# Optimization experiments

Measured on AMD Instinct MI355X. Metric: run time of the kernel, lower is better.

The kernel has to match this reference:

```python
import jax, jax.numpy as jnp
import numpy as np

ALPHA = 0.2  # LeakyReLU negative slope used throughout
NEG = -9e15


def _leaky(x, a=ALPHA):
    return jnp.where(x >= 0, x, a * x)


def _gat_layer(h, adj, W, a, concat):
    # h: [N, Fin], W: [Fin, Fout], a: [2*Fout, 1]
    Wh = h @ W                                   # [N, Fout]
    d = W.shape[-1]
    e = _leaky(Wh @ a[:d] + (Wh @ a[d:]).T)      # [N, N]
    att = jax.nn.softmax(jnp.where(adj > 0, e, NEG), axis=1)
    out = att @ Wh                               # [N, Fout]
    return jax.nn.elu(out) if concat else out


def setup_inputs() -> dict:
    key = jax.random.key(0)
    ks = jax.random.split(key, 24)
    N, F, H, D1, O1 = 4096, 512, 4, 256, 64
    x = jax.random.normal(ks[0], (N, F), dtype=jnp.float32)
    adj = jax.random.bernoulli(ks[1], 0.02, (N, N))
    adj = (adj | adj.T | jnp.eye(N, dtype=bool)).astype(jnp.float32)
    observation = jax.random.randint(ks[2], (1, N), 0, 2, dtype=jnp.int32)
    s_mat = jax.random.uniform(ks[3], (N, N), dtype=jnp.float32)
    theta = jax.random.uniform(ks[4], (1, F), dtype=jnp.float32)
    g = lambda k, s, sc: (jax.random.normal(k, s, dtype=jnp.float32) * sc)
    return {
        'x': x, 'adj': adj, 'observation': observation, 's_mat': s_mat,
        'theta': theta,
        'Wh0': g(ks[5], (H, F, D1), 0.05), 'ah0': g(ks[6], (H, 2 * D1, 1), 0.05),
        'Wh1': g(ks[7], (H, D1, D1), 0.05), 'ah1': g(ks[8], (H, 2 * D1, 1), 0.05),
        'Wo0': g(ks[9], (H * D1, O1), 0.05), 'ao0': g(ks[10], (2 * O1, 1), 0.05),
        'Wo1': g(ks[11], (O1, 1), 0.2), 'ao1': g(ks[12], (2, 1), 0.2),
        'dW': g(ks[13], (2, 10), 0.5), 'dW0': g(ks[14], (1, 10), 0.5),
        'dW1': g(ks[15], (10, 20), 0.5), 'dW01': g(ks[16], (1, 20), 0.5),
        'dW2': g(ks[17], (20, 10), 0.5), 'dW02': g(ks[18], (1, 10), 0.5),
        'dV': g(ks[19], (10, 1), 0.5), 'dV0': g(ks[20], (1, 1), 0.5),
    }


def reference(x, adj, observation, s_mat, theta, Wh0, ah0, Wh1, ah1,
              Wo0, ao0, Wo1, ao1, dW, dW0, dW1, dW01, dW2, dW02, dV, dV0):
    # mergeState: add theta to rows in the seed set (observation[0] == 1)
    seed = (observation[0] == 1).astype(x.dtype)[:, None]  # [N,1]
    h_in = x + seed * theta

    # multi-head 2-layer attention stacks (concat=True -> elu inside)
    def head(W0, a0, W1, a1):
        h = _gat_layer(h_in, adj, W0, a0, True)
        return _gat_layer(h, adj, W1, a1, True)

    hh = jax.vmap(head)(Wh0, ah0, Wh1, ah1)                 # [H, N, D1]
    hcat = jnp.transpose(hh, (1, 0, 2)).reshape(h_in.shape[0], -1)  # [N, H*D1]

    # output attention stack (concat=False), then elu (GAT.forward)
    h = _gat_layer(hcat, adj, Wo0, ao0, False)
    h = _gat_layer(h, adj, Wo1, ao1, False)
    h_ = jax.nn.elu(h)                                      # [N, 1]

    # GAT_degree v2: degreeNN over [h_, degree]
    d_v = s_mat.sum(axis=1, keepdims=True)                  # [N, 1]
    x_ = jnp.concatenate([h_, d_v], axis=1)                 # [N, 2]
    h0 = _leaky(x_ @ dW + dW0)
    h1 = _leaky(h0 @ dW1 + dW01)
    h2 = _leaky(h1 @ dW2 + dW02)
    return _leaky(h2 @ dV + dV0)                            # [N, 1]
```

## Files before the change

kernel.cpp:

```cpp
#include <hip/hip_runtime.h>
#include <hip/hip_bf16.h>
#include <hip/hip_fp16.h>
#include <math.h>

#define MAXDEG 512

typedef short v8s __attribute__((ext_vector_type(8)));
typedef float v4f __attribute__((ext_vector_type(4)));
typedef _Float16 h2 __attribute__((ext_vector_type(2)));

__device__ __forceinline__ float blockReduceSum(float v) {
    __shared__ float sh[8];
    int lane = threadIdx.x & 63, w = threadIdx.x >> 6;
    for (int o = 32; o > 0; o >>= 1) v += __shfl_down(v, o);
    __syncthreads();
    if (lane == 0) sh[w] = v;
    __syncthreads();
    if (w == 0) {
        int nw = (blockDim.x + 63) >> 6;
        v = (lane < nw) ? sh[lane] : 0.f;
        for (int o = 4; o > 0; o >>= 1) v += __shfl_down(v, o);
        if (lane == 0) sh[0] = v;
    }
    __syncthreads();
    return sh[0];
}

__device__ __forceinline__ float blockReduceMax(float v) {
    __shared__ float sh[8];
    int lane = threadIdx.x & 63, w = threadIdx.x >> 6;
    for (int o = 32; o > 0; o >>= 1) v = fmaxf(v, __shfl_down(v, o));
    __syncthreads();
    if (lane == 0) sh[w] = v;
    __syncthreads();
    if (w == 0) {
        int nw = (blockDim.x + 63) >> 6;
        v = (lane < nw) ? sh[lane] : -3.4e38f;
        for (int o = 4; o > 0; o >>= 1) v = fmaxf(v, __shfl_down(v, o));
        if (lane == 0) sh[0] = v;
    }
    __syncthreads();
    return sh[0];
}

__device__ __forceinline__ float leaky(float x) { return x >= 0.f ? x : 0.2f * x; }


__global__ void fused_pre(const float* __restrict__ adj, const float* __restrict__ s,
                          int* __restrict__ colIdx, int* __restrict__ deg,
                          float* __restrict__ dv,
                          const float* __restrict__ x, const int* __restrict__ obs,
                          const float* __restrict__ theta,
                          const float* __restrict__ Wh0, const float* __restrict__ Wh1,
                          const float* __restrict__ Wo0,
                          __half* __restrict__ hin, __half* __restrict__ Wh0t,
                          __half* __restrict__ Wh1t, __half* __restrict__ Wo0t,
                          float* __restrict__ elerZ, int elerN, int N) {
    if (blockIdx.x < 4096) {
        int row = blockIdx.x;
        __shared__ int cnt;
        if (threadIdx.x == 0) cnt = 0;
        __syncthreads();
        const float4* ar = (const float4*)(adj + (size_t)row * N);
        const float4* sr = (const float4*)(s + (size_t)row * N);
        int* outp = colIdx + (size_t)row * MAXDEG;
        float psum = 0.f;
        const int n4 = N >> 2;
        for (int j4 = threadIdx.x; j4 < n4; j4 += blockDim.x) {
            float4 a4 = ar[j4];
            float4 s4 = sr[j4];
            psum += (s4.x + s4.y) + (s4.z + s4.w);
            int jb = j4 << 2;
            if (a4.x > 0.f) { int p = atomicAdd(&cnt, 1); if (p < MAXDEG) outp[p] = jb; }
            if (a4.y > 0.f) { int p = atomicAdd(&cnt, 1); if (p < MAXDEG) outp[p] = jb + 1; }
            if (a4.z > 0.f) { int p = atomicAdd(&cnt, 1); if (p < MAXDEG) outp[p] = jb + 2; }
            if (a4.w > 0.f) { int p = atomicAdd(&cnt, 1); if (p < MAXDEG) outp[p] = jb + 3; }
        }
        psum = blockReduceSum(psum);
        __syncthreads();
        if (threadIdx.x == 0) {
            deg[row] = cnt < MAXDEG ? cnt : MAXDEG;
            dv[row] = psum;
        }
        return;
    }
    const int n0 = 4096 * 512;
    const int n1 = 4 * 512 * 256;
    const int n2 = 4 * 256 * 256;
    const int n3 = 1024 * 64;
    int i = (blockIdx.x - 4096) * 256 + threadIdx.x;
    if (i < n0) {
        int n = i >> 9, f = i & 511;
        float v = x[i];
        if (obs[n] == 1) v += theta[f];
        hin[i] = __float2half(v);
    } else if (i < n0 + n1) {
        int t = i - n0;
        int b = t / (512 * 256), r = t % (512 * 256);
        int mm = r >> 9, kk = r & 511;
        Wh0t[t] = __float2half(Wh0[b * 512 * 256 + kk * 256 + mm]);
    } else if (i < n0 + n1 + n2) {
        int t = i - n0 - n1;
        int b = t >> 16, r = t & 65535;
        int mm = r >> 8, kk = r & 255;
        Wh1t[t] = __float2half(Wh1[b * 65536 + kk * 256 + mm]);
    } else if (i < n0 + n1 + n2 + n3) {
        int t = i - n0 - n1 - n2;
        int mm = t >> 10, kk = t & 1023;
        Wo0t[t] = __float2half(Wo0[kk * 64 + mm]);
    } else if (i < n0 + n1 + n2 + n3 + elerN) {
        elerZ[i - n0 - n1 - n2 - n3] = 0.f;
    }
}

__global__ __launch_bounds__(256) void gemm_mfma128(
    const __half* __restrict__ A, const __half* __restrict__ Bt,
    __half* __restrict__ C, int N, int K, int M,
    size_t sA, size_t sB, size_t sC,
    const float* __restrict__ aVec, size_t aStride,
    float* __restrict__ el, float* __restrict__ er) {
    int b = blockIdx.z;
    const unsigned short* Ag = (const unsigned short*)(A + (size_t)b * sA);
    const unsigned short* Bg = (const unsigned short*)(Bt + (size_t)b * sB);
    __half* Cg = C + (size_t)b * sC;
    const float* av = aVec + (size_t)b * aStride;

    __shared__ __align__(16) unsigned short As[128][40];
    __shared__ __align__(16) unsigned short Bs[128][40];

    const int tid = threadIdx.x;
    const int wave = tid >> 6, lane = tid & 63;
    const int wm = wave >> 1, wn = wave & 1;
    const int row0 = blockIdx.y * 128, col0 = blockIdx.x * 128;
    const int lr = tid >> 2;
    const int lo = (tid & 3) * 8;
    const int m = lane & 15, quad = lane >> 4;

    v4f acc[4][4];
    #pragma unroll
    for (int i = 0; i < 4; i++)
        #pragma unroll
        for (int c = 0; c < 4; c++) acc[i][c] = (v4f)(0.f);

    for (int k0 = 0; k0 < K; k0 += 32) {
        *(int4*)(&As[lr][lo]) =
            *(const int4*)(Ag + (size_t)(row0 + lr) * K + k0 + lo);
        *(int4*)(&As[lr + 64][lo]) =
            *(const int4*)(Ag + (size_t)(row0 + 64 + lr) * K + k0 + lo);
        *(int4*)(&Bs[lr][lo]) =
            *(const int4*)(Bg + (size_t)(col0 + lr) * K + k0 + lo);
        *(int4*)(&Bs[lr + 64][lo]) =
            *(const int4*)(Bg + (size_t)(col0 + 64 + lr) * K + k0 + lo);
        __syncthreads();
        v8s af[4], bfv[4];
        #pragma unroll
        for (int i = 0; i < 4; i++)
            af[i] = *(const v8s*)(&As[wm * 64 + i * 16 + m][quad * 8]);
        #pragma unroll
        for (int c = 0; c < 4; c++)
            bfv[c] = *(const v8s*)(&Bs[wn * 64 + c * 16 + m][quad * 8]);
        #pragma unroll
        for (int i = 0; i < 4; i++)
            #pragma unroll
            for (int c = 0; c < 4; c++)
                acc[i][c] = __builtin_amdgcn_mfma_f32_16x16x32_f16(
                    af[i], bfv[c], acc[i][c], 0, 0, 0);
        __syncthreads();
    }
    #pragma unroll
    for (int i = 0; i < 4; i++)
        #pragma unroll
        for (int c = 0; c < 4; c++)
            #pragma unroll
            for (int r = 0; r < 4; r++) {
                int row = row0 + wm * 64 + i * 16 + quad * 4 + r;
                int col = col0 + wn * 64 + c * 16 + m;
                Cg[(size_t)row * M + col] = __float2half(acc[i][c][r]);
            }
    float ael[4], aer[4];
    #pragma unroll
    for (int c = 0; c < 4; c++) {
        ael[c] = av[col0 + wn * 64 + c * 16 + m];
        aer[c] = av[M + col0 + wn * 64 + c * 16 + m];
    }
    #pragma unroll
    for (int i = 0; i < 4; i++)
        #pragma unroll
        for (int r = 0; r < 4; r++) {
            float pel = 0.f, per_ = 0.f;
            #pragma unroll
            for (int c = 0; c < 4; c++) {
                pel += acc[i][c][r] * ael[c];
                per_ += acc[i][c][r] * aer[c];
            }
            #pragma unroll
            for (int off = 1; off < 16; off <<= 1) {
                pel += __shfl_xor(pel, off);
                per_ += __shfl_xor(per_, off);
            }
            if (m == 0) {
                int row = row0 + wm * 64 + i * 16 + quad * 4 + r;
                atomicAdd(&el[(size_t)b * N + row], pel);
                atomicAdd(&er[(size_t)b * N + row], per_);
            }
        }
}

__global__ __launch_bounds__(256) void gemm_mfma64(
    const __half* __restrict__ A, const __half* __restrict__ Bt,
    __half* __restrict__ C, int N, int K, int M,
    size_t sA, size_t sB, size_t sC,
    const float* __restrict__ aVec, size_t aStride,
    float* __restrict__ el, float* __restrict__ er) {
    int b = blockIdx.z;
    const unsigned short* Ag = (const unsigned short*)(A + (size_t)b * sA);
    const unsigned short* Bg = (const unsigned short*)(Bt + (size_t)b * sB);
    __half* Cg = C + (size_t)b * sC;
    const float* av = aVec + (size_t)b * aStride;

    __shared__ __align__(16) unsigned short As[64][40];
    __shared__ __align__(16) unsigned short Bs[64][40];

    const int tid = threadIdx.x;
    const int wave = tid >> 6, lane = tid & 63;
    const int row0 = blockIdx.y * 64, col0 = blockIdx.x * 64;
    const int sRow = tid >> 2;
    const int sOff = (tid & 3) * 8;
    const int m = lane & 15, quad = lane >> 4;

    v4f acc[4];
    #pragma unroll
    for (int c = 0; c < 4; c++) acc[c] = (v4f)(0.f);

    for (int k0 = 0; k0 < K; k0 += 32) {
        *(int4*)(&As[sRow][sOff]) =
            *(const int4*)(Ag + (size_t)(row0 + sRow) * K + k0 + sOff);
        *(int4*)(&Bs[sRow][sOff]) =
            *(const int4*)(Bg + (size_t)(col0 + sRow) * K + k0 + sOff);
        __syncthreads();
        v8s af = *(const v8s*)(&As[wave * 16 + m][quad * 8]);
        #pragma unroll
        for (int c = 0; c < 4; c++) {
            v8s bfv = *(const v8s*)(&Bs[c * 16 + m][quad * 8]);
            acc[c] = __builtin_amdgcn_mfma_f32_16x16x32_f16(af, bfv, acc[c], 0, 0, 0);
        }
        __syncthreads();
    }
    #pragma unroll
    for (int c = 0; c < 4; c++)
        #pragma unroll
        for (int r = 0; r < 4; r++) {
            int row = row0 + wave * 16 + quad * 4 + r;
            int col = col0 + c * 16 + m;
            Cg[(size_t)row * M + col] = __float2half(acc[c][r]);
        }
    float ael[4], aer[4];
    #pragma unroll
    for (int c = 0; c < 4; c++) {
        ael[c] = av[col0 + c * 16 + m];
        aer[c] = av[M + col0 + c * 16 + m];
    }
    #pragma unroll
    for (int r = 0; r < 4; r++) {
        float pel = 0.f, per_ = 0.f;
        #pragma unroll
        for (int c = 0; c < 4; c++) {
            pel += acc[c][r] * ael[c];
            per_ += acc[c][r] * aer[c];
        }
        #pragma unroll
        for (int off = 1; off < 16; off <<= 1) {
            pel += __shfl_xor(pel, off);
            per_ += __shfl_xor(per_, off);
        }
        if (m == 0) {
            int row = row0 + wave * 16 + quad * 4 + r;
            atomicAdd(&el[(size_t)b * N + row], pel);
            atomicAdd(&er[(size_t)b * N + row], per_);
        }
    }
}

template<int D, int ACT, int HEADS, int FUSE>
__global__ __launch_bounds__(256) void attn_vec(
    const __half* __restrict__ Wh, const float* __restrict__ el,
    const float* __restrict__ er, const int* __restrict__ colIdx,
    const int* __restrict__ deg, __half* __restrict__ out,
    int N, size_t sWh, size_t sOut, int outRowStride,
    const float* __restrict__ wo1, const float* __restrict__ ao1,
    float* __restrict__ o2wh, float* __restrict__ el4, float* __restrict__ er4) {
    constexpr int LPN = D / 8;
    constexpr int SUBS = 64 / LPN;
    constexpr int PER_WAVE = SUBS * 4;
    constexpr int STEP = PER_WAVE * 2;

    const int tid = threadIdx.x;
    const int wave = tid >> 6, lane = tid & 63;
    int b, row;
    if (HEADS == 4) {
        int xcd = blockIdx.x & 7;
        b = xcd >> 1;
        row = ((xcd & 1) << 11) + ((blockIdx.x >> 3) << 2) + wave;
    } else {
        b = 0;
        row = blockIdx.x * 4 + wave;
    }

    const __half* whb = Wh + (size_t)b * sWh;
    const float* erb = er + (size_t)b * N;
    const float eln = el[(size_t)b * N + row];
    const int dc = deg[row];
    const int dcp = (dc + STEP - 1) & ~(STEP - 1);
    const int* ci = colIdx + (size_t)row * MAXDEG;

    __shared__ __align__(16) float2 spc[4][MAXDEG];
    float2* sp = spc[wave];

    float sreg[8];
    int jreg[8];
    float mx = -3.4e38f;
    #pragma unroll
    for (int s8 = 0; s8 < 8; s8++) {
        int k = s8 * 64 + lane;
        if (k < dc) {
            int j = ci[k];
            float s = eln + erb[j];
            s = fmaxf(s, 0.2f * s);
            sreg[s8] = s;
            jreg[s8] = j * (D * 2);
            mx = fmaxf(mx, s);
        }
    }
    #pragma unroll
    for (int off = 1; off < 64; off <<= 1) mx = fmaxf(mx, __shfl_xor(mx, off));

    float l = 0.f;
    #pragma unroll
    for (int s8 = 0; s8 < 8; s8++) {
        int k = s8 * 64 + lane;
        if (k < dc) {
            float p = __expf(sreg[s8] - mx);
            l += p;
            unsigned int pu = __half_as_ushort(__float2half(p));
            sp[k] = make_float2(__int_as_float(pu | (pu << 16)),
                                __int_as_float(jreg[s8]));
        }
    }
    for (int k = dc + lane; k < dcp; k += 64)
        sp[k] = make_float2(__int_as_float(0), __int_as_float(0));
    #pragma unroll
    for (int off = 1; off < 64; off <<= 1) l += __shfl_xor(l, off);
    const float inv = 1.f / l;

    asm volatile("s_waitcnt lgkmcnt(0)" ::: "memory");

    const int sub = lane / LPN;
    const int dl = (lane % LPN) * 8;
    const char* wp = (const char*)(whb + dl);

    union HU { unsigned int u; h2 h; };
    union R4 { uint4 u; h2 h[4]; };

    h2 a0[4], a1[4], a2[4], a3[4];
    #pragma unroll
    for (int i = 0; i < 4; i++) {
        a0[i] = (h2)(_Float16)0; a1[i] = (h2)(_Float16)0;
        a2[i] = (h2)(_Float16)0; a3[i] = (h2)(_Float16)0;
    }

    for (int k = sub * 4; k < dcp; k += STEP) {
        float4 pA = *(const float4*)(&sp[k]);
        float4 pB = *(const float4*)(&sp[k + 2]);
        float4 pC = *(const float4*)(&sp[k + PER_WAVE]);
        float4 pD = *(const float4*)(&sp[k + PER_WAVE + 2]);
        R4 r0, r1, r2, r3, r4, r5, r6, r7;
        r0.u = *(const uint4*)(wp + __float_as_int(pA.y));
        r1.u = *(const uint4*)(wp + __float_as_int(pA.w));
        r2.u = *(const uint4*)(wp + __float_as_int(pB.y));
        r3.u = *(const uint4*)(wp + __float_as_int(pB.w));
        r4.u = *(const uint4*)(wp + __float_as_int(pC.y));
        r5.u = *(const uint4*)(wp + __float_as_int(pC.w));
        r6.u = *(const uint4*)(wp + __float_as_int(pD.y));
        r7.u = *(const uint4*)(wp + __float_as_int(pD.w));
        HU p0, p1, p2, p3, p4, p5, p6, p7;
        p0.u = __float_as_int(pA.x);
        p1.u = __float_as_int(pA.z);
        p2.u = __float_as_int(pB.x);
        p3.u = __float_as_int(pB.z);
        p4.u = __float_as_int(pC.x);
        p5.u = __float_as_int(pC.z);
        p6.u = __float_as_int(pD.x);
        p7.u = __float_as_int(pD.z);
        #pragma unroll
        for (int i = 0; i < 4; i++) {
            a0[i] += p0.h * r0.h[i];
            a1[i] += p2.h * r2.h[i];
            a2[i] += p4.h * r4.h[i];
            a3[i] += p6.h * r6.h[i];
        }
        #pragma unroll
        for (int i = 0; i < 4; i++) {
            a0[i] += p1.h * r1.h[i];
            a1[i] += p3.h * r3.h[i];
            a2[i] += p5.h * r5.h[i];
            a3[i] += p7.h * r7.h[i];
        }
    }
    #pragma unroll
    for (int i = 0; i < 4; i++) a0[i] += (a1[i] + (a2[i] + a3[i]));
    #pragma unroll
    for (int off = LPN; off < 64; off <<= 1)
        #pragma unroll
        for (int i = 0; i < 4; i++) {
            HU t, s;
            t.h = a0[i];
            s.u = __shfl_xor((int)t.u, off);
            a0[i] += s.h;
        }

    if (FUSE) {
        if (sub == 0) {
            float t = 0.f;
            #pragma unroll
            for (int i = 0; i < 4; i++) {
                t += (float)a0[i][0] * inv * wo1[dl + 2 * i];
                t += (float)a0[i][1] * inv * wo1[dl + 2 * i + 1];
            }
            #pragma unroll
            for (int off = 1; off < LPN; off <<= 1) t += __shfl_xor(t, off);
            if (lane == 0) {
                o2wh[row] = t;
                el4[row] = t * ao1[0];
                er4[row] = t * ao1[1];
            }
        }
        return;
    }
    if (sub == 0) {
        __half hv[8];
        #pragma unroll
        for (int i = 0; i < 4; i++) {
            float v0 = (float)a0[i][0] * inv;
            float v1 = (float)a0[i][1] * inv;
            if (ACT == 1) {
                v0 = (v0 > 0.f) ? v0 : expm1f(v0);
                v1 = (v1 > 0.f) ? v1 : expm1f(v1);
            }
            hv[2 * i]     = __float2half(v0);
            hv[2 * i + 1] = __float2half(v1);
        }
        *(uint4*)(out + (size_t)b * sOut + (size_t)row * outRowStride + dl) =
            *(const uint4*)hv;
    }
}

__global__ void attn_d1_deg(const float* __restrict__ o2wh, const float* __restrict__ el,
                            const float* __restrict__ er, const int* __restrict__ colIdx,
                            const int* __restrict__ deg, const float* __restrict__ dv,
                            const float* __restrict__ dW, const float* __restrict__ dW0,
                            const float* __restrict__ dW1, const float* __restrict__ dW01,
                            const float* __restrict__ dW2, const float* __restrict__ dW02,
                            const float* __restrict__ dV, const float* __restrict__ dV0,
                            float* __restrict__ out, int N) {
    int row = blockIdx.x, tid = threadIdx.x;
    const float eln = el[row];
    const int dc = deg[row];
    const int* ci = colIdx + (size_t)row * MAXDEG;
    __shared__ float sp[MAXDEG];
    __shared__ int sc[MAXDEG];
    float mx = -3.4e38f;
    for (int k = tid; k < dc; k += blockDim.x) {
        int j = ci[k];
        sc[k] = j;
        float s = eln + er[j];
        s = fmaxf(s, 0.2f * s);
        sp[k] = s;
        mx = fmaxf(mx, s);
    }
    mx = blockReduceMax(mx);
    float l = 0.f, acc = 0.f;
    for (int k = tid; k < dc; k += blockDim.x) {
        float p = __expf(sp[k] - mx);
        l += p;
        acc += p * o2wh[sc[k]];
    }
    l = blockReduceSum(l);
    acc = blockReduceSum(acc);
    if (tid == 0) {
        float h = acc / l;
        h = (h > 0.f) ? h : expm1f(h);
        float d = dv[row];
        float t0[10], t1[20], t2[10];
        #pragma unroll
        for (int i = 0; i < 10; i++)
            t0[i] = leaky(h * dW[i] + d * dW[10 + i] + dW0[i]);
        #pragma unroll
        for (int j = 0; j < 20; j++) {
            float s = dW01[j];
            #pragma unroll
            for (int i = 0; i < 10; i++) s += t0[i] * dW1[i * 20 + j];
            t1[j] = leaky(s);
        }
        #pragma unroll
        for (int j = 0; j < 10; j++) {
            float s = dW02[j];
            #pragma unroll
            for (int i = 0; i < 20; i++) s += t1[i] * dW2[i * 10 + j];
            t2[j] = leaky(s);
        }
        float o = dV0[0];
        #pragma unroll
        for (int i = 0; i < 10; i++) o += t2[i] * dV[i];
        out[row] = leaky(o);
    }
}

extern "C" void kernel_launch(void* const* d_in, const int* in_sizes, int n_in,
                              void* d_out, int out_size, void* d_ws, size_t ws_size,
                              hipStream_t stream) {
    const int N = 4096, F = 512, H = 4, D1 = 256, O1 = 64;
    const float* x     = (const float*)d_in[0];
    const float* adj   = (const float*)d_in[1];
    const int*   obs   = (const int*)  d_in[2];
    const float* s_mat = (const float*)d_in[3];
    const float* theta = (const float*)d_in[4];
    const float* Wh0   = (const float*)d_in[5];
    const float* ah0   = (const float*)d_in[6];
    const float* Wh1   = (const float*)d_in[7];
    const float* ah1   = (const float*)d_in[8];
    const float* Wo0   = (const float*)d_in[9];
    const float* ao0   = (const float*)d_in[10];
    const float* Wo1   = (const float*)d_in[11];
    const float* ao1   = (const float*)d_in[12];
    const float* dWp   = (const float*)d_in[13];
    const float* dW0p  = (const float*)d_in[14];
    const float* dW1p  = (const float*)d_in[15];
    const float* dW01p = (const float*)d_in[16];
    const float* dW2p  = (const float*)d_in[17];
    const float* dW02p = (const float*)d_in[18];
    const float* dVp   = (const float*)d_in[19];
    const float* dV0p  = (const float*)d_in[20];
    float* outp = (float*)d_out;

    char* ws = (char*)d_ws;
    auto alloc = [&](size_t bytes) {
        char* p = ws;
        ws += (bytes + 255) & ~(size_t)255;
        return p;
    };
    __half* hin  = (__half*)alloc((size_t)N * F * 2);
    __half* whA  = (__half*)alloc((size_t)H * N * D1 * 2);
    __half* hb   = (__half*)alloc((size_t)H * N * D1 * 2);
    __half* hcat = (__half*)alloc((size_t)N * H * D1 * 2);
    __half* o1Wh = (__half*)alloc((size_t)N * O1 * 2);
    float* o2Wh  = (float*)alloc((size_t)N * 4);
    __half* Wh0t = (__half*)alloc((size_t)H * F * D1 * 2);
    __half* Wh1t = (__half*)alloc((size_t)H * D1 * D1 * 2);
    __half* Wo0t = (__half*)alloc((size_t)H * D1 * O1 * 2);
    int elerN = 4 * H * N + 2 * N;
    float* elerZ = (float*)alloc((size_t)elerN * 4);
    float* el1 = elerZ;
    float* er1 = el1 + H * N;
    float* el2 = er1 + H * N;
    float* er2 = el2 + H * N;
    float* el3 = er2 + H * N;
    float* er3 = el3 + N;
    float* el4 = (float*)alloc((size_t)N * 4);
    float* er4 = (float*)alloc((size_t)N * 4);
    float* dv  = (float*)alloc((size_t)N * 4);
    int* colIdx = (int*)alloc((size_t)N * MAXDEG * 4);
    int* deg    = (int*)alloc((size_t)N * 4);

    {
        const int totalPrep = N * F + H * F * D1 + H * D1 * D1 + H * D1 * O1 + elerN;
        const int prepBlocks = (totalPrep + 255) / 256;
        fused_pre<<<4096 + prepBlocks, 256, 0, stream>>>(
            adj, s_mat, colIdx, deg, dv,
            x, obs, theta, Wh0, Wh1, Wo0, hin, Wh0t, Wh1t, Wo0t, elerZ, elerN, N);
    }

    gemm_mfma128<<<dim3(D1 / 128, N / 128, H), 256, 0, stream>>>(
        hin, Wh0t, whA, N, F, D1, 0, (size_t)D1 * F, (size_t)N * D1,
        ah0, (size_t)2 * D1, el1, er1);
    attn_vec<256, 1, 4, 0><<<(N * H) / 4, 256, 0, stream>>>(
        whA, el1, er1, colIdx, deg, hb,
        N, (size_t)N * D1, (size_t)N * D1, D1,
        nullptr, nullptr, nullptr, nullptr, nullptr);

    gemm_mfma128<<<dim3(D1 / 128, N / 128, H), 256, 0, stream>>>(
        hb, Wh1t, whA, N, D1, D1, (size_t)N * D1, (size_t)D1 * D1, (size_t)N * D1,
        ah1, (size_t)2 * D1, el2, er2);
    attn_vec<256, 1, 4, 0><<<(N * H) / 4, 256, 0, stream>>>(
        whA, el2, er2, colIdx, deg, hcat,
        N, (size_t)N * D1, (size_t)D1, H * D1,
        nullptr, nullptr, nullptr, nullptr, nullptr);

    gemm_mfma64<<<dim3(O1 / 64, N / 64, 1), 256, 0, stream>>>(
        hcat, Wo0t, o1Wh, N, H * D1, O1, 0, 0, 0,
        ao0, 0, el3, er3);
    attn_vec<64, 0, 1, 1><<<N / 4, 256, 0, stream>>>(
        o1Wh, el3, er3, colIdx, deg, nullptr,
        N, 0, 0, O1,
        Wo1, ao1, o2Wh, el4, er4);

    attn_d1_deg<<<N, 256, 0, stream>>>(o2Wh, el4, er4, colIdx, deg, dv,
        dWp, dW0p, dW1p, dW01p, dW2p, dW02p, dVp, dV0p, outp, N);
}
```

Measured before the change: 389.9 us.

## Use 64x128 GEMM tiles and LDS-tiled weight transposes in prep kernel

The head GEMMs switch from 128x128 to 64x128 block tiles. Each wave now computes 16 rows by 128 columns, and the grid doubles in the row dimension, which raises block count and occupancy for these fairly small GEMMs. The weight transpose-and-convert in the prep kernel moves from strided per-element gathers to 64x64 shared-memory tiles with coalesced float4 loads and 16-byte half stores. The trade-off is less A/B reuse per block, plus extra el/er atomics because each block now covers fewer columns per row.

```diff
diff --git a/kernel.cpp b/kernel.cpp
--- a/kernel.cpp
+++ b/kernel.cpp
@@ -56,17 +56,18 @@
                           __half* __restrict__ hin, __half* __restrict__ Wh0t,
                           __half* __restrict__ Wh1t, __half* __restrict__ Wo0t,
                           float* __restrict__ elerZ, int elerN, int N) {
+    const int tid = threadIdx.x;
     if (blockIdx.x < 4096) {
         int row = blockIdx.x;
         __shared__ int cnt;
-        if (threadIdx.x == 0) cnt = 0;
+        if (tid == 0) cnt = 0;
         __syncthreads();
         const float4* ar = (const float4*)(adj + (size_t)row * N);
         const float4* sr = (const float4*)(s + (size_t)row * N);
         int* outp = colIdx + (size_t)row * MAXDEG;
         float psum = 0.f;
         const int n4 = N >> 2;
-        for (int j4 = threadIdx.x; j4 < n4; j4 += blockDim.x) {
+        for (int j4 = tid; j4 < n4; j4 += blockDim.x) {
             float4 a4 = ar[j4];
             float4 s4 = sr[j4];
             psum += (s4.x + s4.y) + (s4.z + s4.w);
@@ -78,42 +79,73 @@
         }
         psum = blockReduceSum(psum);
         __syncthreads();
-        if (threadIdx.x == 0) {
+        if (tid == 0) {
             deg[row] = cnt < MAXDEG ? cnt : MAXDEG;
             dv[row] = psum;
         }
         return;
     }
-    const int n0 = 4096 * 512;
-    const int n1 = 4 * 512 * 256;
-    const int n2 = 4 * 256 * 256;
-    const int n3 = 1024 * 64;
-    int i = (blockIdx.x - 4096) * 256 + threadIdx.x;
-    if (i < n0) {
+    int bb = blockIdx.x - 4096;
+    if (bb < 8192) {
+        int i = bb * 256 + tid;
         int n = i >> 9, f = i & 511;
         float v = x[i];
         if (obs[n] == 1) v += theta[f];
         hin[i] = __float2half(v);
-    } else if (i < n0 + n1) {
-        int t = i - n0;
-        int b = t / (512 * 256), r = t % (512 * 256);
-        int mm = r >> 9, kk = r & 511;
-        Wh0t[t] = __float2half(Wh0[b * 512 * 256 + kk * 256 + mm]);
-    } else if (i < n0 + n1 + n2) {
-        int t = i - n0 - n1;
-        int b = t >> 16, r = t & 65535;
-        int mm = r >> 8, kk = r & 255;
-        Wh1t[t] = __float2half(Wh1[b * 65536 + kk * 256 + mm]);
-    } else if (i < n0 + n1 + n2 + n3) {
-        int t = i - n0 - n1 - n2;
-        int mm = t >> 10, kk = t & 1023;
-        Wo0t[t] = __float2half(Wo0[kk * 64 + mm]);
-    } else if (i < n0 + n1 + n2 + n3 + elerN) {
-        elerZ[i - n0 - n1 - n2 - n3] = 0.f;
-    }
-}
-
-__global__ __launch_bounds__(256) void gemm_mfma128(
+        return;
+    }
+    bb -= 8192;
+    if (bb < 288) {
+        int i = bb * 256 + tid;
+        if (i < elerN) elerZ[i] = 0.f;
+        return;
+    }
+    int t = bb - 288;
+    const float* src;
+    __half* dst;
+    int srcStride, dstStride;
+    if (t < 128) {
+        int b = t >> 5, tt = t & 31, kt = tt >> 2, mt = tt & 3;
+        src = Wh0 + b * 131072 + (kt * 64) * 256 + mt * 64;
+        dst = Wh0t + b * 131072 + (mt * 64) * 512 + kt * 64;
+        srcStride = 256; dstStride = 512;
+    } else if (t < 192) {
+        int u = t - 128;
+        int b = u >> 4, tt = u & 15, kt = tt >> 2, mt = tt & 3;
+        src = Wh1 + b * 65536 + (kt * 64) * 256 + mt * 64;
+        dst = Wh1t + b * 65536 + (mt * 64) * 256 + kt * 64;
+        srcStride = 256; dstStride = 256;
+    } else {
+        int kt = t - 192;
+        src = Wo0 + (kt * 64) * 64;
+        dst = Wo0t + kt * 64;
+        srcStride = 64; dstStride = 1024;
+    }
+    __shared__ float tile[64][65];
+    int rr = tid >> 4;
+    int cc = (tid & 15) * 4;
+    #pragma unroll
+    for (int sI = 0; sI < 4; sI++) {
+        float4 v = *(const float4*)(src + (size_t)(rr + sI * 16) * srcStride + cc);
+        tile[rr + sI * 16][cc]     = v.x;
+        tile[rr + sI * 16][cc + 1] = v.y;
+        tile[rr + sI * 16][cc + 2] = v.z;
+        tile[rr + sI * 16][cc + 3] = v.w;
+    }
+    __syncthreads();
+    int mr = tid >> 2;
+    int kc = (tid & 3) * 16;
+    #pragma unroll
+    for (int g = 0; g < 2; g++) {
+        v8s v;
+        #pragma unroll
+        for (int e = 0; e < 8; e++)
+            v[e] = (short)__half_as_ushort(__float2half(tile[kc + g * 8 + e][mr]));
+        *(v8s*)(dst + (size_t)mr * dstStride + kc + g * 8) = v;
+    }
+}
+
+__global__ __launch_bounds__(256) void gemm_mfma64x128(
     const __half* __restrict__ A, const __half* __restrict__ Bt,
     __half* __restrict__ C, int N, int K, int M,
     size_t sA, size_t sB, size_t sC,
@@ -125,85 +157,69 @@
     __half* Cg = C + (size_t)b * sC;
     const float* av = aVec + (size_t)b * aStride;
 
-    __shared__ __align__(16) unsigned short As[128][40];
+    __shared__ __align__(16) unsigned short As[64][40];
     __shared__ __align__(16) unsigned short Bs[128][40];
 
     const int tid = threadIdx.x;
     const int wave = tid >> 6, lane = tid & 63;
-    const int wm = wave >> 1, wn = wave & 1;
-    const int row0 = blockIdx.y * 128, col0 = blockIdx.x * 128;
+    const int row0 = blockIdx.y * 64, col0 = blockIdx.x * 128;
     const int lr = tid >> 2;
     const int lo = (tid & 3) * 8;
     const int m = lane & 15, quad = lane >> 4;
 
-    v4f acc[4][4];
-    #pragma unroll
-    for (int i = 0; i < 4; i++)
-        #pragma unroll
-        for (int c = 0; c < 4; c++) acc[i][c] = (v4f)(0.f);
+    v4f acc[8];
+    #pragma unroll
+    for (int c = 0; c < 8; c++) acc[c] = (v4f)(0.f);
 
     for (int k0 = 0; k0 < K; k0 += 32) {
         *(int4*)(&As[lr][lo]) =
             *(const int4*)(Ag + (size_t)(row0 + lr) * K + k0 + lo);
-        *(int4*)(&As[lr + 64][lo]) =
-            *(const int4*)(Ag + (size_t)(row0 + 64 + lr) * K + k0 + lo);
         *(int4*)(&Bs[lr][lo]) =
             *(const int4*)(Bg + (size_t)(col0 + lr) * K + k0 + lo);
         *(int4*)(&Bs[lr + 64][lo]) =
             *(const int4*)(Bg + (size_t)(col0 + 64 + lr) * K + k0 + lo);
         __syncthreads();
-        v8s af[4], bfv[4];
-        #pragma unroll
-        for (int i = 0; i < 4; i++)
-            af[i] = *(const v8s*)(&As[wm * 64 + i * 16 + m][quad * 8]);
-        #pragma unroll
-        for (int c = 0; c < 4; c++)
-            bfv[c] = *(const v8s*)(&Bs[wn * 64 + c * 16 + m][quad * 8]);
-        #pragma unroll
-        for (int i = 0; i < 4; i++)
-            #pragma unroll
-            for (int c = 0; c < 4; c++)
-                acc[i][c] = __builtin_amdgcn_mfma_f32_16x16x32_f16(
-                    af[i], bfv[c], acc[i][c], 0, 0, 0);
+        v8s af = *(const v8s*)(&As[wave * 16 + m][quad * 8]);
+        #pragma unroll
+        for (int c = 0; c < 8; c++) {
+            v8s bfv = *(const v8s*)(&Bs[c * 16 + m][quad * 8]);
+            acc[c] = __builtin_amdgcn_mfma_f32_16x16x32_f16(af, bfv, acc[c], 0, 0, 0);
+        }
         __syncthreads();
     }
     #pragma unroll
-    for (int i = 0; i < 4; i++)
-        #pragma unroll
-        for (int c = 0; c < 4; c++)
-            #pragma unroll
-            for (int r = 0; r < 4; r++) {
-                int row = row0 + wm * 64 + i * 16 + quad * 4 + r;
-                int col = col0 + wn * 64 + c * 16 + m;
-                Cg[(size_t)row * M + col] = __float2half(acc[i][c][r]);
-            }
-    float ael[4], aer[4];
-    #pragma unroll
-    for (int c = 0; c < 4; c++) {
-        ael[c] = av[col0 + wn * 64 + c * 16 + m];
-        aer[c] = av[M + col0 + wn * 64 + c * 16 + m];
-    }
-    #pragma unroll
-    for (int i = 0; i < 4; i++)
+    for (int c = 0; c < 8; c++)
         #pragma unroll
         for (int r = 0; r < 4; r++) {
-            float pel = 0.f, per_ = 0.f;
-            #pragma unroll
-            for (int c = 0; c < 4; c++) {
-                pel += acc[i][c][r] * ael[c];
-                per_ += acc[i][c][r] * aer[c];
-            }
-            #pragma unroll
-            for (int off = 1; off < 16; off <<= 1) {
-                pel += __shfl_xor(pel, off);
-                per_ += __shfl_xor(per_, off);
-            }
-            if (m == 0) {
-                int row = row0 + wm * 64 + i * 16 + quad * 4 + r;
-                atomicAdd(&el[(size_t)b * N + row], pel);
-                atomicAdd(&er[(size_t)b * N + row], per_);
-            }
-        }
+            int row = row0 + wave * 16 + quad * 4 + r;
+            int col = col0 + c * 16 + m;
+            Cg[(size_t)row * M + col] = __float2half(acc[c][r]);
+        }
+    float ael[8], aer[8];
+    #pragma unroll
+    for (int c = 0; c < 8; c++) {
+        ael[c] = av[col0 + c * 16 + m];
+        aer[c] = av[M + col0 + c * 16 + m];
+    }
+    #pragma unroll
+    for (int r = 0; r < 4; r++) {
+        float pel = 0.f, per_ = 0.f;
+        #pragma unroll
+        for (int c = 0; c < 8; c++) {
+            pel += acc[c][r] * ael[c];
+            per_ += acc[c][r] * aer[c];
+        }
+        #pragma unroll
+        for (int off = 1; off < 16; off <<= 1) {
+            pel += __shfl_xor(pel, off);
+            per_ += __shfl_xor(per_, off);
+        }
+        if (m == 0) {
+            int row = row0 + wave * 16 + quad * 4 + r;
+            atomicAdd(&el[(size_t)b * N + row], pel);
+            atomicAdd(&er[(size_t)b * N + row], per_);
+        }
+    }
 }
 
 __global__ __launch_bounds__(256) void gemm_mfma64(
@@ -572,14 +588,12 @@
     int* deg    = (int*)alloc((size_t)N * 4);
 
     {
-        const int totalPrep = N * F + H * F * D1 + H * D1 * D1 + H * D1 * O1 + elerN;
-        const int prepBlocks = (totalPrep + 255) / 256;
-        fused_pre<<<4096 + prepBlocks, 256, 0, stream>>>(
+        fused_pre<<<4096 + 8192 + 288 + 208, 256, 0, stream>>>(
             adj, s_mat, colIdx, deg, dv,
             x, obs, theta, Wh0, Wh1, Wo0, hin, Wh0t, Wh1t, Wo0t, elerZ, elerN, N);
     }
 
-    gemm_mfma128<<<dim3(D1 / 128, N / 128, H), 256, 0, stream>>>(
+    gemm_mfma64x128<<<dim3(D1 / 128, N / 64, H), 256, 0, stream>>>(
         hin, Wh0t, whA, N, F, D1, 0, (size_t)D1 * F, (size_t)N * D1,
         ah0, (size_t)2 * D1, el1, er1);
     attn_vec<256, 1, 4, 0><<<(N * H) / 4, 256, 0, stream>>>(
@@ -587,7 +601,7 @@
         N, (size_t)N * D1, (size_t)N * D1, D1,
         nullptr, nullptr, nullptr, nullptr, nullptr);
 
-    gemm_mfma128<<<dim3(D1 / 128, N / 128, H), 256, 0, stream>>>(
+    gemm_mfma64x128<<<dim3(D1 / 128, N / 64, H), 256, 0, stream>>>(
         hb, Wh1t, whA, N, D1, D1, (size_t)N * D1, (size_t)D1 * D1, (size_t)N * D1,
         ah1, (size_t)2 * D1, el2, er2);
     attn_vec<256, 1, 4, 0><<<(N * H) / 4, 256, 0, stream>>>(
```

Result: no change. 385.2 us (-1.2%).
